# Kernel tuning notes

Hardware: AMD Instinct MI355X
Metric: run time of the kernel (lower is better)

The kernel has to match this reference:

```python
import jax, jax.numpy as jnp
import numpy as np

B, T, F, D = 8, 2048, 512, 256

def setup_inputs() -> dict:
    key = jax.random.key(0)
    k1, k2, k3, k4 = jax.random.split(key, 4)
    scale = 1.0 / np.sqrt(F)
    return {
        "inputs": jax.random.normal(k1, (B, T, F), dtype=jnp.float32),
        "W_q": jax.random.normal(k2, (F, D), dtype=jnp.float32) * scale,
        "W_k": jax.random.normal(k3, (F, D), dtype=jnp.float32) * scale,
        "W_v": jax.random.normal(k4, (F, D), dtype=jnp.float32) * scale,
    }

def reference(inputs, W_q, W_k, W_v):
    # Q,K,V: [B,T,D]
    Q = jnp.einsum('btf,fd->btd', inputs, W_q)
    K = jnp.einsum('btf,fd->btd', inputs, W_k)
    V = jnp.einsum('btf,fd->btd', inputs, W_v)
    d = Q.shape[-1]
    scores = jnp.einsum('bqd,bkd->bqk', Q, K) / jnp.sqrt(jnp.asarray(d, dtype=Q.dtype))
    attn = jax.nn.softmax(scores, axis=-1)  # [B,T,T]
    return jnp.einsum('bqk,bkd->bqd', attn, V)
```

## Files before the change

kernel.cpp:

```cpp
#include <hip/hip_runtime.h>
#include <cstdint>
#include <cstddef>

#define B_ 8
#define T_ 2048
#define F_ 512
#define D_ 256
#define NSPLIT 2
#define KVB 32
#define NT ((T_ / NSPLIT) / KVB)

typedef float f32x4 __attribute__((ext_vector_type(4)));
typedef __bf16 bf16x8 __attribute__((ext_vector_type(8)));
typedef unsigned short us8 __attribute__((ext_vector_type(8)));
typedef unsigned short us4 __attribute__((ext_vector_type(4)));

static __device__ __forceinline__ unsigned short f2bf(float f) {
  union { float f; unsigned int u; } v; v.f = f;
  unsigned int u = v.u;
  u += 0x7fffu + ((u >> 16) & 1u);
  return (unsigned short)(u >> 16);
}

static __device__ __forceinline__ float bf2f(unsigned short s) {
  union { float f; unsigned int u; } v; v.u = ((unsigned int)s) << 16;
  return v.f;
}

static __device__ __forceinline__ bf16x8 ldb8(const unsigned short* p) {
  return *reinterpret_cast<const bf16x8*>(p);
}

static __device__ __forceinline__ f32x4 mfma_bf16(bf16x8 a, bf16x8 b, f32x4 c) {
  return __builtin_amdgcn_mfma_f32_16x16x32_bf16(a, b, c, 0, 0, 0);
}

static __device__ __forceinline__ void gload_lds16(const unsigned short* g,
                                                   unsigned short* l) {
  __builtin_amdgcn_global_load_lds(
      (const __attribute__((address_space(1))) void*)g,
      (__attribute__((address_space(3))) void*)l, 16, 0, 0);
}

__global__ __launch_bounds__(256) void xb_kernel(const float* __restrict__ X,
                                                 unsigned short* __restrict__ Xb) {
  size_t i = ((size_t)blockIdx.x * 256 + threadIdx.x) * 8;
  float4 a = *reinterpret_cast<const float4*>(&X[i]);
  float4 b = *reinterpret_cast<const float4*>(&X[i + 4]);
  us8 p;
  p[0] = f2bf(a.x); p[1] = f2bf(a.y); p[2] = f2bf(a.z); p[3] = f2bf(a.w);
  p[4] = f2bf(b.x); p[5] = f2bf(b.y); p[6] = f2bf(b.z); p[7] = f2bf(b.w);
  *reinterpret_cast<us8*>(&Xb[i]) = p;
}

__global__ __launch_bounds__(256) void tw_kernel(const float* __restrict__ Wq,
                                                 const float* __restrict__ Wk,
                                                 const float* __restrict__ Wv,
                                                 unsigned short* __restrict__ Wt) {
  __shared__ unsigned short tile[64][72];
  const float* W = (blockIdx.z == 0) ? Wq : (blockIdx.z == 1) ? Wk : Wv;
  unsigned short* out = Wt + (size_t)blockIdx.z * (D_ * F_);
  int k0 = blockIdx.x * 64, n0 = blockIdx.y * 64;
  int t = threadIdx.x;
#pragma unroll
  for (int i = 0; i < 4; i++) {
    int c = t + 256 * i;
    int r = c >> 4, c4 = (c & 15) * 4;
    float4 v = *reinterpret_cast<const float4*>(&W[(size_t)(k0 + r) * D_ + n0 + c4]);
    us4 p; p[0] = f2bf(v.x); p[1] = f2bf(v.y); p[2] = f2bf(v.z); p[3] = f2bf(v.w);
    *reinterpret_cast<us4*>(&tile[r][c4]) = p;
  }
  __syncthreads();
#pragma unroll
  for (int i = 0; i < 4; i++) {
    int c = t + 256 * i;
    int r = c >> 4, c4 = (c & 15) * 4;
    us4 p;
    p[0] = tile[c4 + 0][r];
    p[1] = tile[c4 + 1][r];
    p[2] = tile[c4 + 2][r];
    p[3] = tile[c4 + 3][r];
    *reinterpret_cast<us4*>(&out[(size_t)(n0 + r) * F_ + k0 + c4]) = p;
  }
}

__global__ __launch_bounds__(256) void proj_kernel(const unsigned short* __restrict__ Xb,
                                                   const unsigned short* __restrict__ Wt,
                                                   unsigned short* __restrict__ Qs,
                                                   unsigned short* __restrict__ Kb,
                                                   unsigned short* __restrict__ Vt) {
  __shared__ unsigned short Au[2][128 * 64];
  __shared__ unsigned short Bu[2][128 * 64];
  const int brow = blockIdx.x * 128;
  const int bcol = blockIdx.y * 128;
  const int z = blockIdx.z;
  const unsigned short* W = Wt + (size_t)z * (D_ * F_);
  const int tid = threadIdx.x;
  const int wave = tid >> 6, lane = tid & 63;
  const int wr = wave >> 1, wc = wave & 1;
  const int lg = lane >> 4, lr = lane & 15;

  f32x4 acc[4][4] = {};

  auto stageT = [&](unsigned short* dst, const unsigned short* srcBase, int k0) {
#pragma unroll
    for (int i = 0; i < 4; i++) {
      int L = (tid + 256 * i) * 16;
      int r = L >> 7;
      int c = L & 127;
      int csw = c ^ ((r & 7) << 4);
      gload_lds16(srcBase + (size_t)r * F_ + k0 + (csw >> 1), dst + (L >> 1));
    }
  };

  stageT(Au[0], Xb + (size_t)brow * F_, 0);
  stageT(Bu[0], W + (size_t)bcol * F_, 0);
  __syncthreads();

  for (int ks = 0; ks < 8; ks++) {
    const int cur = ks & 1;
    if (ks + 1 < 8) {
      stageT(Au[cur ^ 1], Xb + (size_t)brow * F_, (ks + 1) * 64);
      stageT(Bu[cur ^ 1], W + (size_t)bcol * F_, (ks + 1) * 64);
    }
#pragma unroll
    for (int kk = 0; kk < 2; kk++) {
      bf16x8 af[4], bfr[4];
#pragma unroll
      for (int mi = 0; mi < 4; mi++) {
        int r = wr * 64 + mi * 16 + lr;
        af[mi] = ldb8(&Au[cur][r * 64 + ((((kk * 64 + lg * 16) ^ ((r & 7) << 4))) >> 1)]);
      }
#pragma unroll
      for (int ni = 0; ni < 4; ni++) {
        int r = wc * 64 + ni * 16 + lr;
        bfr[ni] = ldb8(&Bu[cur][r * 64 + ((((kk * 64 + lg * 16) ^ ((r & 7) << 4))) >> 1)]);
      }
#pragma unroll
      for (int mi = 0; mi < 4; mi++)
#pragma unroll
        for (int ni = 0; ni < 4; ni++)
          acc[mi][ni] = mfma_bf16(af[mi], bfr[ni], acc[mi][ni]);
    }
    __syncthreads();
  }

#pragma unroll
  for (int mi = 0; mi < 4; mi++) {
#pragma unroll
    for (int ni = 0; ni < 4; ni++) {
      int row0 = brow + wr * 64 + mi * 16 + lg * 4;
      int col = bcol + wc * 64 + ni * 16 + lr;
      if (z == 0) {
#pragma unroll
        for (int j = 0; j < 4; j++)
          Qs[(size_t)(row0 + j) * D_ + col] = f2bf(acc[mi][ni][j] * 0.09016844f);
      } else if (z == 1) {
#pragma unroll
        for (int j = 0; j < 4; j++)
          Kb[(size_t)(row0 + j) * D_ + col] = f2bf(acc[mi][ni][j]);
      } else {
        int b = row0 >> 11, t0 = row0 & (T_ - 1);
        us4 p;
#pragma unroll
        for (int j = 0; j < 4; j++) p[j] = f2bf(acc[mi][ni][j]);
        *reinterpret_cast<us4*>(&Vt[(size_t)b * D_ * T_ + (size_t)col * T_ + t0]) = p;
      }
    }
  }
}

__global__ __launch_bounds__(256)
void flash_kernel(const unsigned short* __restrict__ Qs,
                  const unsigned short* __restrict__ Kb,
                  const unsigned short* __restrict__ Vt,
                  unsigned short* __restrict__ op,
                  float2* __restrict__ ml) {
  __shared__ unsigned short Kl[2][KVB * 256];
  __shared__ unsigned short Vl[2][256 * KVB];
  __shared__ unsigned short Pl[4][16][40];

  const int b = blockIdx.x, qt = blockIdx.y, h = blockIdx.z;
  const int tid = threadIdx.x;
  const int wave = tid >> 6, lane = tid & 63;
  const int lg = lane >> 4, lr = lane & 15;

  const int qrow = qt * 64 + wave * 16 + lr;
  const unsigned short* qptr = Qs + ((size_t)b * T_ + qrow) * D_;
  bf16x8 qf[8];
#pragma unroll
  for (int ks = 0; ks < 8; ks++) qf[ks] = ldb8(qptr + ks * 32 + lg * 8);

  f32x4 o[16] = {};
  float m = -__builtin_inff();
  float lsum = 0.f;

  const int keyoff = h * (T_ / NSPLIT);
  const unsigned short* kbase = Kb + (size_t)b * T_ * D_ + (size_t)keyoff * D_;
  const unsigned short* vbase = Vt + (size_t)b * D_ * T_;

  auto stage = [&](int buf, int kt) {
    const unsigned short* ksrc = kbase + (size_t)kt * KVB * D_;
#pragma unroll
    for (int i = 0; i < 4; i++) {
      int L = (tid + 256 * i) * 16;
      int r = L >> 9;
      int c = L & 511;
      int csw = c ^ ((r & 7) << 4);
      gload_lds16(ksrc + r * 256 + (csw >> 1), &Kl[buf][L >> 1]);
    }
    const int key0 = keyoff + kt * KVB;
#pragma unroll
    for (int i = 0; i < 4; i++) {
      int idx = tid + 256 * i;
      int kg = idx >> 8;
      int d = (idx & 255) ^ (kg << 1);
      gload_lds16(vbase + (size_t)d * T_ + key0 + kg * 8, &Vl[buf][idx * 8]);
    }
  };

  stage(0, 0);
  __syncthreads();

  for (int kt = 0; kt < NT; kt++) {
    const int cur = kt & 1;
    if (kt + 1 < NT) stage(cur ^ 1, kt + 1);

    f32x4 s[2] = {};
    __builtin_amdgcn_s_setprio(1);
#pragma unroll
    for (int ks = 0; ks < 8; ks++) {
#pragma unroll
      for (int nf = 0; nf < 2; nf++) {
        int r = nf * 16 + lr;
        bf16x8 kb = ldb8(&Kl[cur][r * 256 + (((ks * 64 + lg * 16) ^ ((r & 7) << 4)) >> 1)]);
        s[nf] = mfma_bf16(kb, qf[ks], s[nf]);
      }
    }
    __builtin_amdgcn_s_setprio(0);

    float pm;
    {
      float a0 = fmaxf(fmaxf(s[0][0], s[0][1]), fmaxf(s[0][2], s[0][3]));
      float a1 = fmaxf(fmaxf(s[1][0], s[1][1]), fmaxf(s[1][2], s[1][3]));
      pm = fmaxf(a0, a1);
      pm = fmaxf(pm, __shfl_xor(pm, 16));
      pm = fmaxf(pm, __shfl_xor(pm, 32));
    }
    if (!__all(pm - m <= 8.0f)) {
      float mn = fmaxf(m, pm);
      float corr = exp2f(m - mn);
      m = mn;
      lsum *= corr;
      float c4[4];
#pragma unroll
      for (int j = 0; j < 4; j++) c4[j] = __shfl(corr, lg * 4 + j);
#pragma unroll
      for (int nf = 0; nf < 16; nf++)
#pragma unroll
        for (int j = 0; j < 4; j++) o[nf][j] *= c4[j];
    }
    float rs = 0.f;
#pragma unroll
    for (int nf = 0; nf < 2; nf++) {
      us4 pk;
#pragma unroll
      for (int j = 0; j < 4; j++) {
        float p = exp2f(s[nf][j] - m);
        rs += p;
        pk[j] = f2bf(p);
      }
      *reinterpret_cast<us4*>(&Pl[wave][lr][nf * 16 + lg * 4]) = pk;
    }
    rs += __shfl_xor(rs, 16);
    rs += __shfl_xor(rs, 32);
    lsum += rs;

    __builtin_amdgcn_s_setprio(1);
    {
      bf16x8 pa = ldb8(&Pl[wave][lr][lg * 8]);
#pragma unroll
      for (int nf = 0; nf < 16; nf++) {
        int d = nf * 16 + lr;
        bf16x8 vb = ldb8(&Vl[cur][(lg << 11) + (((d ^ (lg << 1)) & 255) << 3)]);
        o[nf] = mfma_bf16(pa, vb, o[nf]);
      }
    }
    __builtin_amdgcn_s_setprio(0);

    __syncthreads();
  }

  const size_t rowbase = (size_t)h * (B_ * T_) + (size_t)b * T_;
#pragma unroll
  for (int nf = 0; nf < 16; nf++) {
#pragma unroll
    for (int j = 0; j < 4; j++) {
      int q = qt * 64 + wave * 16 + lg * 4 + j;
      op[(rowbase + q) * D_ + nf * 16 + lr] = f2bf(o[nf][j]);
    }
  }
  if (lg == 0) {
    int q = qt * 64 + wave * 16 + lr;
    ml[rowbase + q] = make_float2(m, lsum);
  }
}

__global__ __launch_bounds__(256) void merge_kernel(const unsigned short* __restrict__ op,
                                                    const float2* __restrict__ ml,
                                                    float* __restrict__ out) {
  const int tid = threadIdx.x;
  const int row = blockIdx.x * 4 + (tid >> 6);
  const int d0 = (tid & 63) * 4;

  float mh[NSPLIT], lh[NSPLIT];
  float M = -__builtin_inff();
#pragma unroll
  for (int hh = 0; hh < NSPLIT; hh++) {
    float2 v = ml[(size_t)hh * (B_ * T_) + row];
    mh[hh] = v.x; lh[hh] = v.y;
    M = fmaxf(M, v.x);
  }
  float e[NSPLIT], den = 0.f;
#pragma unroll
  for (int hh = 0; hh < NSPLIT; hh++) {
    e[hh] = exp2f(mh[hh] - M);
    den += e[hh] * lh[hh];
  }
  const float inv = 1.0f / den;

  float acc[4] = {0.f, 0.f, 0.f, 0.f};
#pragma unroll
  for (int hh = 0; hh < NSPLIT; hh++) {
    us4 p = *reinterpret_cast<const us4*>(
        &op[((size_t)hh * (B_ * T_) + row) * D_ + d0]);
#pragma unroll
    for (int j = 0; j < 4; j++) acc[j] += e[hh] * bf2f(p[j]);
  }
  float4 r;
  r.x = acc[0] * inv; r.y = acc[1] * inv; r.z = acc[2] * inv; r.w = acc[3] * inv;
  *reinterpret_cast<float4*>(&out[(size_t)row * D_ + d0]) = r;
}

extern "C" void kernel_launch(void* const* d_in, const int* in_sizes, int n_in,
                              void* d_out, int out_size, void* d_ws, size_t ws_size,
                              hipStream_t stream) {
  const float* X  = (const float*)d_in[0];
  const float* Wq = (const float*)d_in[1];
  const float* Wk = (const float*)d_in[2];
  const float* Wv = (const float*)d_in[3];
  float* out = (float*)d_out;

  char* ws = (char*)d_ws;
  unsigned short* Wt = (unsigned short*)ws;
  unsigned short* Qs = (unsigned short*)(ws + 786432);
  unsigned short* Kb = (unsigned short*)(ws + 786432 + 8388608);
  unsigned short* Vt = (unsigned short*)(ws + 786432 + 2 * 8388608);
  unsigned short* op = (unsigned short*)(ws + 786432 + 3 * 8388608);
  unsigned short* Xb = op;
  float2* ml        = (float2*)(ws + 786432 + 3 * 8388608 + (size_t)NSPLIT * B_ * T_ * D_ * 2);

  xb_kernel<<<dim3((B_ * T_ * F_) / (256 * 8)), 256, 0, stream>>>(X, Xb);
  tw_kernel<<<dim3(F_ / 64, D_ / 64, 3), 256, 0, stream>>>(Wq, Wk, Wv, Wt);
  proj_kernel<<<dim3((B_ * T_) / 128, D_ / 128, 3), 256, 0, stream>>>(Xb, Wt, Qs, Kb, Vt);
  flash_kernel<<<dim3(B_, T_ / 64, NSPLIT), 256, 0, stream>>>(Qs, Kb, Vt, op, ml);
  merge_kernel<<<dim3(B_ * T_ / 4), 256, 0, stream>>>(op, ml, out);
}
```

Baseline: 118.5 us.

## Use 16-key KV tiles with 16x16x16 MFMA to keep P in registers

Cuts the KV tile from 32 to 16 keys and raises the split-K factor from 2 to 4. The P fragment produced by the QK^T MFMA can then feed a 16x16x16 bf16 MFMA directly from registers, which removes the per-wave LDS round trip for P. Launch bounds now request 4 blocks per SM. In exchange the kernel runs twice as many iterations, each ending in a block barrier, the PV matmul uses a smaller MFMA shape, and the merge kernel has more partial results to combine.

```diff
diff --git a/kernel.cpp b/kernel.cpp
--- a/kernel.cpp
+++ b/kernel.cpp
@@ -6,12 +6,13 @@
 #define T_ 2048
 #define F_ 512
 #define D_ 256
-#define NSPLIT 2
-#define KVB 32
+#define NSPLIT 4
+#define KVB 16
 #define NT ((T_ / NSPLIT) / KVB)
 
 typedef float f32x4 __attribute__((ext_vector_type(4)));
 typedef __bf16 bf16x8 __attribute__((ext_vector_type(8)));
+typedef short s16x4 __attribute__((ext_vector_type(4)));
 typedef unsigned short us8 __attribute__((ext_vector_type(8)));
 typedef unsigned short us4 __attribute__((ext_vector_type(4)));
 
@@ -33,6 +34,21 @@
 
 static __device__ __forceinline__ f32x4 mfma_bf16(bf16x8 a, bf16x8 b, f32x4 c) {
   return __builtin_amdgcn_mfma_f32_16x16x32_bf16(a, b, c, 0, 0, 0);
+}
+
+#if defined(__has_builtin)
+#if __has_builtin(__builtin_amdgcn_mfma_f32_16x16x16bf16_1k)
+#define HAVE_MFMA16 1
+#endif
+#endif
+static __device__ __forceinline__ f32x4 mfma16(us4 a, us4 b, f32x4 c) {
+#ifdef HAVE_MFMA16
+  return __builtin_amdgcn_mfma_f32_16x16x16bf16_1k((s16x4)a, (s16x4)b, c, 0, 0, 0);
+#else
+  asm volatile("v_mfma_f32_16x16x16_bf16 %0, %1, %2, %0"
+               : "+v"(c) : "v"(a), "v"(b));
+  return c;
+#endif
 }
 
 static __device__ __forceinline__ void gload_lds16(const unsigned short* g,
@@ -170,7 +186,7 @@
   }
 }
 
-__global__ __launch_bounds__(256)
+__global__ __launch_bounds__(256, 4)
 void flash_kernel(const unsigned short* __restrict__ Qs,
                   const unsigned short* __restrict__ Kb,
                   const unsigned short* __restrict__ Vt,
@@ -178,7 +194,6 @@
                   float2* __restrict__ ml) {
   __shared__ unsigned short Kl[2][KVB * 256];
   __shared__ unsigned short Vl[2][256 * KVB];
-  __shared__ unsigned short Pl[4][16][40];
 
   const int b = blockIdx.x, qt = blockIdx.y, h = blockIdx.z;
   const int tid = threadIdx.x;
@@ -202,20 +217,20 @@
   auto stage = [&](int buf, int kt) {
     const unsigned short* ksrc = kbase + (size_t)kt * KVB * D_;
 #pragma unroll
-    for (int i = 0; i < 4; i++) {
-      int L = (tid + 256 * i) * 16;
-      int r = L >> 9;
-      int c = L & 511;
-      int csw = c ^ ((r & 7) << 4);
-      gload_lds16(ksrc + r * 256 + (csw >> 1), &Kl[buf][L >> 1]);
+    for (int i = 0; i < 2; i++) {
+      int idx = tid + 256 * i;
+      int r = idx >> 5;
+      int cb = (idx & 31) << 4;
+      int csw = cb ^ ((r & 7) << 4);
+      gload_lds16(ksrc + r * 256 + (csw >> 1), &Kl[buf][idx * 8]);
     }
     const int key0 = keyoff + kt * KVB;
 #pragma unroll
-    for (int i = 0; i < 4; i++) {
+    for (int i = 0; i < 2; i++) {
       int idx = tid + 256 * i;
-      int kg = idx >> 8;
-      int d = (idx & 255) ^ (kg << 1);
-      gload_lds16(vbase + (size_t)d * T_ + key0 + kg * 8, &Vl[buf][idx * 8]);
+      int d = idx >> 1;
+      int h2 = idx & 1;
+      gload_lds16(vbase + (size_t)d * T_ + key0 + h2 * 8, &Vl[buf][idx * 8]);
     }
   };
 
@@ -226,27 +241,18 @@
     const int cur = kt & 1;
     if (kt + 1 < NT) stage(cur ^ 1, kt + 1);
 
-    f32x4 s[2] = {};
+    f32x4 s = {};
     __builtin_amdgcn_s_setprio(1);
 #pragma unroll
     for (int ks = 0; ks < 8; ks++) {
-#pragma unroll
-      for (int nf = 0; nf < 2; nf++) {
-        int r = nf * 16 + lr;
-        bf16x8 kb = ldb8(&Kl[cur][r * 256 + (((ks * 64 + lg * 16) ^ ((r & 7) << 4)) >> 1)]);
-        s[nf] = mfma_bf16(kb, qf[ks], s[nf]);
-      }
+      bf16x8 kb = ldb8(&Kl[cur][lr * 256 + (((ks * 64 + lg * 16) ^ ((lr & 7) << 4)) >> 1)]);
+      s = mfma_bf16(kb, qf[ks], s);
     }
     __builtin_amdgcn_s_setprio(0);
 
-    float pm;
-    {
-      float a0 = fmaxf(fmaxf(s[0][0], s[0][1]), fmaxf(s[0][2], s[0][3]));
-      float a1 = fmaxf(fmaxf(s[1][0], s[1][1]), fmaxf(s[1][2], s[1][3]));
-      pm = fmaxf(a0, a1);
-      pm = fmaxf(pm, __shfl_xor(pm, 16));
-      pm = fmaxf(pm, __shfl_xor(pm, 32));
-    }
+    float pm = fmaxf(fmaxf(s[0], s[1]), fmaxf(s[2], s[3]));
+    pm = fmaxf(pm, __shfl_xor(pm, 16));
+    pm = fmaxf(pm, __shfl_xor(pm, 32));
     if (!__all(pm - m <= 8.0f)) {
       float mn = fmaxf(m, pm);
       float corr = exp2f(m - mn);
@@ -260,36 +266,32 @@
 #pragma unroll
         for (int j = 0; j < 4; j++) o[nf][j] *= c4[j];
     }
+    us4 pk;
     float rs = 0.f;
 #pragma unroll
-    for (int nf = 0; nf < 2; nf++) {
-      us4 pk;
-#pragma unroll
-      for (int j = 0; j < 4; j++) {
-        float p = exp2f(s[nf][j] - m);
-        rs += p;
-        pk[j] = f2bf(p);
-      }
-      *reinterpret_cast<us4*>(&Pl[wave][lr][nf * 16 + lg * 4]) = pk;
+    for (int j = 0; j < 4; j++) {
+      float p = exp2f(s[j] - m);
+      rs += p;
+      pk[j] = f2bf(p);
     }
     rs += __shfl_xor(rs, 16);
     rs += __shfl_xor(rs, 32);
     lsum += rs;
 
     __builtin_amdgcn_s_setprio(1);
-    {
-      bf16x8 pa = ldb8(&Pl[wave][lr][lg * 8]);
-#pragma unroll
-      for (int nf = 0; nf < 16; nf++) {
-        int d = nf * 16 + lr;
-        bf16x8 vb = ldb8(&Vl[cur][(lg << 11) + (((d ^ (lg << 1)) & 255) << 3)]);
-        o[nf] = mfma_bf16(pa, vb, o[nf]);
-      }
+#pragma unroll
+    for (int nf = 0; nf < 16; nf++) {
+      us4 vb = *reinterpret_cast<const us4*>(&Vl[cur][(nf * 16 + lr) * 16 + lg * 4]);
+      o[nf] = mfma16(pk, vb, o[nf]);
     }
     __builtin_amdgcn_s_setprio(0);
 
     __syncthreads();
   }
+
+#ifndef HAVE_MFMA16
+  asm volatile("s_nop 7\n\ts_nop 7" ::: );
+#endif
 
   const size_t rowbase = (size_t)h * (B_ * T_) + (size_t)b * T_;
 #pragma unroll
```

New measurement: 145.7 us. 1.23x slower.
